# Performance work log

Hardware: AMD Instinct MI355X
Metric: run time of the kernel (lower is better)

## Reference

```python
import jax, jax.numpy as jnp
import numpy as np

N_NODES = 200000
N_EDGES = 6400000
IN_DIM = 15      # pfc_input_dim
POS_DIM = 4      # positional_dim
OUT_DIM = 2      # vtx_classes + 1


def setup_inputs() -> dict:
    key = jax.random.key(0)
    k1, k2, k3, k4, k5, k6, k7 = jax.random.split(key, 7)
    x_pfc = jax.random.normal(k1, (N_NODES, IN_DIM), dtype=jnp.float32)
    edge_index = jax.random.randint(k2, (2, N_EDGES), 0, N_NODES, dtype=jnp.int64)
    s_in = 1.0 / np.sqrt(IN_DIM)
    s_pos = 1.0 / np.sqrt(POS_DIM)
    # PointTransformerConv params: lin, lin_src, lin_dst (no bias), pos_nn = Linear(4, 2)
    W_lin = jax.random.uniform(k3, (OUT_DIM, IN_DIM), jnp.float32, -s_in, s_in)
    W_src = jax.random.uniform(k4, (OUT_DIM, IN_DIM), jnp.float32, -s_in, s_in)
    W_dst = jax.random.uniform(k5, (OUT_DIM, IN_DIM), jnp.float32, -s_in, s_in)
    W_pos = jax.random.uniform(k6, (OUT_DIM, POS_DIM), jnp.float32, -s_pos, s_pos)
    b_pos = jax.random.uniform(k7, (OUT_DIM,), jnp.float32, -s_pos, s_pos)
    return {"x_pfc": x_pfc, "edge_index": edge_index, "W_lin": W_lin,
            "W_src": W_src, "W_dst": W_dst, "W_pos": W_pos, "b_pos": b_pos}


def reference(x_pfc, edge_index, W_lin, W_src, W_dst, W_pos, b_pos):
    n = x_pfc.shape[0]
    pos = x_pfc[:, :POS_DIM]
    # original forward calls ptc_only(x, pos, edge_index.flip(0)):
    # source j = edge_index[1], target i = edge_index[0]
    j = edge_index[1]
    i = edge_index[0]
    # node-level linear maps (N x OUT_DIM)
    v = x_pfc @ W_lin.T
    a_src = x_pfc @ W_src.T
    a_dst = x_pfc @ W_dst.T
    # positional MLP on relative positions (E x OUT_DIM)
    delta = (pos[i] - pos[j]) @ W_pos.T + b_pos
    alpha = a_dst[i] - a_src[j] + delta
    # segment softmax over incoming edges of each target node i
    m = jax.ops.segment_max(alpha, i, num_segments=n)  # -inf for empty segments (never indexed)
    e = jnp.exp(alpha - m[i])
    denom = jax.ops.segment_sum(e, i, num_segments=n)
    attn = e / (denom[i] + 1e-16)
    msg = attn * (v[j] + delta)
    return jax.ops.segment_sum(msg, i, num_segments=n)
```

## Files before the change

### kernel.cpp

```cpp
#include <hip/hip_runtime.h>

#define N_NODES 200000
#define N_EDGES 6400000
#define IN_DIM 15
#define POS_DIM 4

#define CSHIFT 9
#define CMASK 511
#define NCOARSE ((N_NODES + 511) >> 9)
#define CHUNK 12288
#define NBLK ((N_EDGES + CHUNK - 1) / CHUNK)
#define CAP 17408

typedef unsigned uv4 __attribute__((ext_vector_type(4)));
typedef int      iv4 __attribute__((ext_vector_type(4)));


__global__ void node_prep(const float* __restrict__ x,
                          const float* __restrict__ Wlin,
                          const float* __restrict__ Wsrc,
                          const float* __restrict__ Wpos,
                          float4* __restrict__ tabJ,
                          unsigned* __restrict__ gcnt)
{
    int n = blockIdx.x * blockDim.x + threadIdx.x;
    if (n < NCOARSE) gcnt[n] = 0u;
    if (n >= N_NODES) return;
    const float* xp = x + (long)n * IN_DIM;
    float xv[IN_DIM];
#pragma unroll
    for (int k = 0; k < IN_DIM; ++k) xv[k] = xp[k];

    float p0 = 0.f, p1 = 0.f;
#pragma unroll
    for (int k = 0; k < POS_DIM; ++k) {
        p0 += Wpos[k] * xv[k];
        p1 += Wpos[POS_DIM + k] * xv[k];
    }
    float v0 = 0.f, v1 = 0.f, as0 = 0.f, as1 = 0.f;
#pragma unroll
    for (int k = 0; k < IN_DIM; ++k) {
        float xk = xv[k];
        v0  += Wlin[k] * xk;  v1  += Wlin[IN_DIM + k] * xk;
        as0 += Wsrc[k] * xk;  as1 += Wsrc[IN_DIM + k] * xk;
    }
    tabJ[n] = make_float4(as0 + p0, as1 + p1, v0 - p0, v1 - p1);
}

__global__ __launch_bounds__(512) void
scatter_kernel(const int* __restrict__ idx,
               unsigned* __restrict__ gcnt,
               unsigned* __restrict__ packed)
{
    __shared__ unsigned stage[CHUNK];
    __shared__ unsigned cnt[512];
    __shared__ unsigned gdst[NCOARSE];
    __shared__ unsigned wsum[8];
    int b = blockIdx.x;
    int t = threadIdx.x;
    int lane = t & 63, wid = t >> 6;
    long s0 = (long)b * CHUNK;
    int end = (int)min((long)CHUNK, (long)N_EDGES - s0);
    cnt[t] = 0u;
    __syncthreads();
    iv4 myi[6];
    {
        int rr = 0;
        for (int e = t * 4; e < end; e += 2048, ++rr) {
            iv4 iv = *(const iv4*)(idx + s0 + e);
            myi[rr] = iv;
            atomicAdd(&cnt[iv.x >> CSHIFT], 1u);
            atomicAdd(&cnt[iv.y >> CSHIFT], 1u);
            atomicAdd(&cnt[iv.z >> CSHIFT], 1u);
            atomicAdd(&cnt[iv.w >> CSHIFT], 1u);
        }
    }
    __syncthreads();
    unsigned v = cnt[t];
    unsigned s = v;
#pragma unroll
    for (int off = 1; off < 64; off <<= 1) {
        unsigned u = __shfl_up(s, off, 64);
        if (lane >= off) s += u;
    }
    if (lane == 63) wsum[wid] = s;
    __syncthreads();
    unsigned woff = 0;
#pragma unroll
    for (int w = 0; w < 8; ++w) woff += (w < wid) ? wsum[w] : 0u;
    {
        unsigned ex = woff + s - v;
        cnt[t] = ex;
        if (t < NCOARSE) gdst[t] = atomicAdd(&gcnt[t], v);
    }
    __syncthreads();
    {
        int rr = 0;
        for (int e = t * 4; e < end; e += 2048, ++rr) {
            iv4 iv = myi[rr];
            iv4 jv = *(const iv4*)(idx + N_EDGES + s0 + e);
            unsigned r0 = atomicAdd(&cnt[iv.x >> CSHIFT], 1u);
            unsigned r1 = atomicAdd(&cnt[iv.y >> CSHIFT], 1u);
            unsigned r2 = atomicAdd(&cnt[iv.z >> CSHIFT], 1u);
            unsigned r3 = atomicAdd(&cnt[iv.w >> CSHIFT], 1u);
            stage[r0] = ((unsigned)jv.x << CSHIFT) | ((unsigned)iv.x & CMASK);
            stage[r1] = ((unsigned)jv.y << CSHIFT) | ((unsigned)iv.y & CMASK);
            stage[r2] = ((unsigned)jv.z << CSHIFT) | ((unsigned)iv.z & CMASK);
            stage[r3] = ((unsigned)jv.w << CSHIFT) | ((unsigned)iv.w & CMASK);
        }
    }
    __syncthreads();
    for (int bk = wid; bk < NCOARSE; bk += 8) {
        unsigned st  = bk ? cnt[bk - 1] : 0u;
        unsigned len = cnt[bk] - st;
        unsigned gb  = gdst[bk];
        unsigned rem = (gb < (unsigned)CAP) ? (unsigned)CAP - gb : 0u;
        if (len > rem) len = rem;
        unsigned* dst = packed + (size_t)bk * CAP + gb;
        for (unsigned e = lane; e < len; e += 64u)
            dst[e] = stage[st + e];
    }
}

__global__ __launch_bounds__(1024) void
bucket_agg_kernel(const unsigned* __restrict__ packed,
                  const unsigned* __restrict__ gcnt,
                  const float* __restrict__ x,
                  const float* __restrict__ Wdst,
                  const float* __restrict__ Wpos,
                  const float4* __restrict__ tabJ,
                  const float* __restrict__ bpos,
                  float2* __restrict__ out)
{
    __shared__ unsigned cache[CAP + 512];
    __shared__ unsigned cnt[512], cur[512];
    __shared__ unsigned wsum[8];
    int k = blockIdx.x;
    int t = threadIdx.x;
    int lane = t & 63;
    int r = t >> 1, sub = t & 1;
    float b0 = bpos[0], b1 = bpos[1];
    int gn = (k << CSHIFT) + r;

    float p0 = 0.f, p1 = 0.f, ad0 = 0.f, ad1 = 0.f;
    if (gn < N_NODES) {
        const float* xp = x + (long)gn * IN_DIM;
        float xv[IN_DIM];
#pragma unroll
        for (int q = 0; q < IN_DIM; ++q) xv[q] = xp[q];
#pragma unroll
        for (int q = 0; q < POS_DIM; ++q) {
            p0 += Wpos[q] * xv[q];
            p1 += Wpos[POS_DIM + q] * xv[q];
        }
#pragma unroll
        for (int q = 0; q < IN_DIM; ++q) {
            ad0 += Wdst[q] * xv[q];
            ad1 += Wdst[IN_DIM + q] * xv[q];
        }
    }
    float a0 = ad0 + p0 + b0, a1 = ad1 + p1 + b1;
    float sn0 = 0.f, sn1 = 0.f, sd0 = 0.f, sd1 = 0.f;

    if (t < 512) cnt[t] = 0u;
    __syncthreads();

    unsigned n = min(gcnt[k], (unsigned)CAP);
    const unsigned* pk = packed + (size_t)k * CAP;

    for (unsigned e = 4u * t; e < n; e += 4096u) {
        uv4 p = *(const uv4*)(pk + e);
        atomicAdd(&cnt[p.x & CMASK], 1u);
        if (e + 1 < n) atomicAdd(&cnt[p.y & CMASK], 1u);
        if (e + 2 < n) atomicAdd(&cnt[p.z & CMASK], 1u);
        if (e + 3 < n) atomicAdd(&cnt[p.w & CMASK], 1u);
    }
    __syncthreads();
    unsigned v = 0, s = 0;
    if (t < 512) {
        v = cnt[t];
        s = v;
#pragma unroll
        for (int off = 1; off < 64; off <<= 1) {
            unsigned u = __shfl_up(s, off, 64);
            if (lane >= off) s += u;
        }
        if (lane == 63) wsum[t >> 6] = s;
    }
    __syncthreads();
    if (t < 512) {
        int wid = t >> 6;
        unsigned woff = 0;
#pragma unroll
        for (int w = 0; w < 8; ++w) woff += (w < wid) ? wsum[w] : 0u;
        cur[t] = woff + s - v + (unsigned)t;
    }
    __syncthreads();
    for (unsigned e = 4u * t; e < n; e += 4096u) {
        uv4 p = __builtin_nontemporal_load((const uv4*)(pk + e));
        { unsigned pos = atomicAdd(&cur[p.x & CMASK], 1u); cache[pos] = p.x >> CSHIFT; }
        if (e + 1 < n) { unsigned pos = atomicAdd(&cur[p.y & CMASK], 1u); cache[pos] = p.y >> CSHIFT; }
        if (e + 2 < n) { unsigned pos = atomicAdd(&cur[p.z & CMASK], 1u); cache[pos] = p.z >> CSHIFT; }
        if (e + 3 < n) { unsigned pos = atomicAdd(&cur[p.w & CMASK], 1u); cache[pos] = p.w >> CSHIFT; }
    }
    __syncthreads();
    unsigned deg   = cnt[r];
    unsigned st    = cur[r] - deg;
    unsigned half0 = (deg + 1) >> 1;
    unsigned myst  = st + (sub ? half0 : 0u);
    unsigned mylen = sub ? (deg - half0) : half0;
    unsigned e = 0;
    for (; e + 8u <= mylen; e += 8u) {
        unsigned j0 = cache[myst + e],     j1 = cache[myst + e + 1];
        unsigned j2 = cache[myst + e + 2], j3 = cache[myst + e + 3];
        unsigned j4 = cache[myst + e + 4], j5 = cache[myst + e + 5];
        unsigned j6 = cache[myst + e + 6], j7 = cache[myst + e + 7];
        float4 f0 = tabJ[j0], f1 = tabJ[j1], f2 = tabJ[j2], f3 = tabJ[j3];
        float4 f4 = tabJ[j4], f5 = tabJ[j5], f6 = tabJ[j6], f7 = tabJ[j7];
        float e00 = __expf(a0 - f0.x), e01 = __expf(a1 - f0.y);
        float e10 = __expf(a0 - f1.x), e11 = __expf(a1 - f1.y);
        float e20 = __expf(a0 - f2.x), e21 = __expf(a1 - f2.y);
        float e30 = __expf(a0 - f3.x), e31 = __expf(a1 - f3.y);
        float e40 = __expf(a0 - f4.x), e41 = __expf(a1 - f4.y);
        float e50 = __expf(a0 - f5.x), e51 = __expf(a1 - f5.y);
        float e60 = __expf(a0 - f6.x), e61 = __expf(a1 - f6.y);
        float e70 = __expf(a0 - f7.x), e71 = __expf(a1 - f7.y);
        sn0 += e00 * f0.z + e10 * f1.z + e20 * f2.z + e30 * f3.z
             + e40 * f4.z + e50 * f5.z + e60 * f6.z + e70 * f7.z;
        sn1 += e01 * f0.w + e11 * f1.w + e21 * f2.w + e31 * f3.w
             + e41 * f4.w + e51 * f5.w + e61 * f6.w + e71 * f7.w;
        sd0 += e00 + e10 + e20 + e30 + e40 + e50 + e60 + e70;
        sd1 += e01 + e11 + e21 + e31 + e41 + e51 + e61 + e71;
    }
    for (; e < mylen; ++e) {
        unsigned j = cache[myst + e];
        float4 fj = tabJ[j];
        float e0 = __expf(a0 - fj.x), e1 = __expf(a1 - fj.y);
        sn0 += e0 * fj.z;  sn1 += e1 * fj.w;
        sd0 += e0;         sd1 += e1;
    }
    sn0 += __shfl_xor(sn0, 1);  sn1 += __shfl_xor(sn1, 1);
    sd0 += __shfl_xor(sd0, 1);  sd1 += __shfl_xor(sd1, 1);

    if (sub != 0 || gn >= N_NODES) return;
    float o0 = (sn0 + (p0 + b0) * sd0) / (sd0 + 1e-16f);
    float o1 = (sn1 + (p1 + b1) * sd1) / (sd1 + 1e-16f);
    out[gn] = make_float2(o0, o1);
}

extern "C" void kernel_launch(void* const* d_in, const int* in_sizes, int n_in,
                              void* d_out, int out_size, void* d_ws, size_t ws_size,
                              hipStream_t stream) {
    const float* x    = (const float*)d_in[0];
    const int*   idx  = (const int*)d_in[1];
    const float* Wlin = (const float*)d_in[2];
    const float* Wsrc = (const float*)d_in[3];
    const float* Wdst = (const float*)d_in[4];
    const float* Wpos = (const float*)d_in[5];
    const float* bpos = (const float*)d_in[6];
    float* out = (float*)d_out;

    char* ws = (char*)d_ws;
    size_t off = 0;
    float4* tabJ = (float4*)(ws + off); off += (size_t)N_NODES * 16;
    unsigned* packed = (unsigned*)(ws + off); off += (size_t)NCOARSE * CAP * 4;
    unsigned* gcnt   = (unsigned*)(ws + off); off += (size_t)NCOARSE * 4;

    node_prep<<<(N_NODES + 255) / 256, 256, 0, stream>>>(x, Wlin, Wsrc, Wpos,
                                                         tabJ, gcnt);
    scatter_kernel<<<NBLK, 512, 0, stream>>>(idx, gcnt, packed);
    bucket_agg_kernel<<<NCOARSE, 1024, 0, stream>>>(packed, gcnt,
                                                    x, Wdst, Wpos, tabJ, bpos,
                                                    (float2*)out);
}
```

Before: 164.8 us.

## Fuse node projection into scatter kernel and precompute destination-side table

Removes the separate node_prep kernel by computing per-node projections inside the scatter kernel, with each of the 521 blocks handling 384 nodes before its edge binning. It also precomputes a destination-side table (a_dst plus the positional term and bias) so the aggregation kernel reads one float4 instead of recomputing from x. The flush loop now gives each half-wave its own bucket, and gcnt is cleared with a memset. The trade-offs are an extra 3.2MB table write, added register pressure in the scatter kernel, and still one extra launch from the memset.

```diff
diff --git a/kernel.cpp b/kernel.cpp
--- a/kernel.cpp
+++ b/kernel.cpp
@@ -11,46 +11,24 @@
 #define CHUNK 12288
 #define NBLK ((N_EDGES + CHUNK - 1) / CHUNK)
 #define CAP 17408
+#define NPB 384
 
 typedef unsigned uv4 __attribute__((ext_vector_type(4)));
 typedef int      iv4 __attribute__((ext_vector_type(4)));
 
 
-__global__ void node_prep(const float* __restrict__ x,
-                          const float* __restrict__ Wlin,
-                          const float* __restrict__ Wsrc,
-                          const float* __restrict__ Wpos,
-                          float4* __restrict__ tabJ,
-                          unsigned* __restrict__ gcnt)
-{
-    int n = blockIdx.x * blockDim.x + threadIdx.x;
-    if (n < NCOARSE) gcnt[n] = 0u;
-    if (n >= N_NODES) return;
-    const float* xp = x + (long)n * IN_DIM;
-    float xv[IN_DIM];
-#pragma unroll
-    for (int k = 0; k < IN_DIM; ++k) xv[k] = xp[k];
-
-    float p0 = 0.f, p1 = 0.f;
-#pragma unroll
-    for (int k = 0; k < POS_DIM; ++k) {
-        p0 += Wpos[k] * xv[k];
-        p1 += Wpos[POS_DIM + k] * xv[k];
-    }
-    float v0 = 0.f, v1 = 0.f, as0 = 0.f, as1 = 0.f;
-#pragma unroll
-    for (int k = 0; k < IN_DIM; ++k) {
-        float xk = xv[k];
-        v0  += Wlin[k] * xk;  v1  += Wlin[IN_DIM + k] * xk;
-        as0 += Wsrc[k] * xk;  as1 += Wsrc[IN_DIM + k] * xk;
-    }
-    tabJ[n] = make_float4(as0 + p0, as1 + p1, v0 - p0, v1 - p1);
-}
-
 __global__ __launch_bounds__(512) void
-scatter_kernel(const int* __restrict__ idx,
+scatter_kernel(const float* __restrict__ x,
+               const float* __restrict__ Wlin,
+               const float* __restrict__ Wsrc,
+               const float* __restrict__ Wdst,
+               const float* __restrict__ Wpos,
+               const float* __restrict__ bpos,
+               const int* __restrict__ idx,
                unsigned* __restrict__ gcnt,
-               unsigned* __restrict__ packed)
+               unsigned* __restrict__ packed,
+               float4* __restrict__ tabJ,
+               float4* __restrict__ tabI4)
 {
     __shared__ unsigned stage[CHUNK];
     __shared__ unsigned cnt[512];
@@ -61,6 +39,34 @@
     int lane = t & 63, wid = t >> 6;
     long s0 = (long)b * CHUNK;
     int end = (int)min((long)CHUNK, (long)N_EDGES - s0);
+
+    {
+        int nb = b * NPB + t;
+        if (t < NPB && nb < N_NODES) {
+            const float* xp = x + (long)nb * IN_DIM;
+            float xv[IN_DIM];
+#pragma unroll
+            for (int q = 0; q < IN_DIM; ++q) xv[q] = xp[q];
+            float p0 = 0.f, p1 = 0.f;
+#pragma unroll
+            for (int q = 0; q < POS_DIM; ++q) {
+                p0 += Wpos[q] * xv[q];
+                p1 += Wpos[POS_DIM + q] * xv[q];
+            }
+            float v0 = 0.f, v1 = 0.f, as0 = 0.f, as1 = 0.f, ad0 = 0.f, ad1 = 0.f;
+#pragma unroll
+            for (int q = 0; q < IN_DIM; ++q) {
+                float xk = xv[q];
+                v0  += Wlin[q] * xk;  v1  += Wlin[IN_DIM + q] * xk;
+                as0 += Wsrc[q] * xk;  as1 += Wsrc[IN_DIM + q] * xk;
+                ad0 += Wdst[q] * xk;  ad1 += Wdst[IN_DIM + q] * xk;
+            }
+            float b0 = bpos[0], b1 = bpos[1];
+            tabJ[nb]  = make_float4(as0 + p0, as1 + p1, v0 - p0, v1 - p1);
+            tabI4[nb] = make_float4(ad0 + p0 + b0, ad1 + p1 + b1, p0 + b0, p1 + b1);
+        }
+    }
+
     cnt[t] = 0u;
     __syncthreads();
     iv4 myi[6];
@@ -110,26 +116,26 @@
         }
     }
     __syncthreads();
-    for (int bk = wid; bk < NCOARSE; bk += 8) {
-        unsigned st  = bk ? cnt[bk - 1] : 0u;
-        unsigned len = cnt[bk] - st;
-        unsigned gb  = gdst[bk];
-        unsigned rem = (gb < (unsigned)CAP) ? (unsigned)CAP - gb : 0u;
-        if (len > rem) len = rem;
-        unsigned* dst = packed + (size_t)bk * CAP + gb;
-        for (unsigned e = lane; e < len; e += 64u)
-            dst[e] = stage[st + e];
+    {
+        int h = lane >> 5, lane32 = lane & 31;
+        for (int bk = wid * 2 + h; bk < NCOARSE; bk += 16) {
+            unsigned st  = bk ? cnt[bk - 1] : 0u;
+            unsigned len = cnt[bk] - st;
+            unsigned gb  = gdst[bk];
+            unsigned rem = (gb < (unsigned)CAP) ? (unsigned)CAP - gb : 0u;
+            if (len > rem) len = rem;
+            unsigned* dst = packed + (size_t)bk * CAP + gb;
+            for (unsigned e = lane32; e < len; e += 32u)
+                dst[e] = stage[st + e];
+        }
     }
 }
 
 __global__ __launch_bounds__(1024) void
 bucket_agg_kernel(const unsigned* __restrict__ packed,
                   const unsigned* __restrict__ gcnt,
-                  const float* __restrict__ x,
-                  const float* __restrict__ Wdst,
-                  const float* __restrict__ Wpos,
                   const float4* __restrict__ tabJ,
-                  const float* __restrict__ bpos,
+                  const float4* __restrict__ tabI4,
                   float2* __restrict__ out)
 {
     __shared__ unsigned cache[CAP + 512];
@@ -139,27 +145,11 @@
     int t = threadIdx.x;
     int lane = t & 63;
     int r = t >> 1, sub = t & 1;
-    float b0 = bpos[0], b1 = bpos[1];
     int gn = (k << CSHIFT) + r;
 
-    float p0 = 0.f, p1 = 0.f, ad0 = 0.f, ad1 = 0.f;
-    if (gn < N_NODES) {
-        const float* xp = x + (long)gn * IN_DIM;
-        float xv[IN_DIM];
-#pragma unroll
-        for (int q = 0; q < IN_DIM; ++q) xv[q] = xp[q];
-#pragma unroll
-        for (int q = 0; q < POS_DIM; ++q) {
-            p0 += Wpos[q] * xv[q];
-            p1 += Wpos[POS_DIM + q] * xv[q];
-        }
-#pragma unroll
-        for (int q = 0; q < IN_DIM; ++q) {
-            ad0 += Wdst[q] * xv[q];
-            ad1 += Wdst[IN_DIM + q] * xv[q];
-        }
-    }
-    float a0 = ad0 + p0 + b0, a1 = ad1 + p1 + b1;
+    float4 ai = make_float4(0.f, 0.f, 0.f, 0.f);
+    if (gn < N_NODES) ai = tabI4[gn];
+    float a0 = ai.x, a1 = ai.y;
     float sn0 = 0.f, sn1 = 0.f, sd0 = 0.f, sd1 = 0.f;
 
     if (t < 512) cnt[t] = 0u;
@@ -243,8 +233,8 @@
     sd0 += __shfl_xor(sd0, 1);  sd1 += __shfl_xor(sd1, 1);
 
     if (sub != 0 || gn >= N_NODES) return;
-    float o0 = (sn0 + (p0 + b0) * sd0) / (sd0 + 1e-16f);
-    float o1 = (sn1 + (p1 + b1) * sd1) / (sd1 + 1e-16f);
+    float o0 = (sn0 + ai.z * sd0) / (sd0 + 1e-16f);
+    float o1 = (sn1 + ai.w * sd1) / (sd1 + 1e-16f);
     out[gn] = make_float2(o0, o1);
 }
 
@@ -262,14 +252,14 @@
 
     char* ws = (char*)d_ws;
     size_t off = 0;
-    float4* tabJ = (float4*)(ws + off); off += (size_t)N_NODES * 16;
+    float4* tabJ  = (float4*)(ws + off); off += (size_t)N_NODES * 16;
+    float4* tabI4 = (float4*)(ws + off); off += (size_t)N_NODES * 16;
     unsigned* packed = (unsigned*)(ws + off); off += (size_t)NCOARSE * CAP * 4;
     unsigned* gcnt   = (unsigned*)(ws + off); off += (size_t)NCOARSE * 4;
 
-    node_prep<<<(N_NODES + 255) / 256, 256, 0, stream>>>(x, Wlin, Wsrc, Wpos,
-                                                         tabJ, gcnt);
-    scatter_kernel<<<NBLK, 512, 0, stream>>>(idx, gcnt, packed);
+    hipMemsetAsync(gcnt, 0, (size_t)NCOARSE * sizeof(unsigned), stream);
+    scatter_kernel<<<NBLK, 512, 0, stream>>>(x, Wlin, Wsrc, Wdst, Wpos, bpos,
+                                             idx, gcnt, packed, tabJ, tabI4);
     bucket_agg_kernel<<<NCOARSE, 1024, 0, stream>>>(packed, gcnt,
-                                                    x, Wdst, Wpos, tabJ, bpos,
-                                                    (float2*)out);
+                                                    tabJ, tabI4, (float2*)out);
 }
```

After: 163.4 us. No clear change (-0.9%).
